# Optimization experiments

Measured on AMD Instinct MI355X. Metric: run time of the kernel, lower is better.

Reference implementation:

```python
import jax, jax.numpy as jnp
import numpy as np

N = 64           # protein_length
B = 32           # batch
L = 2 * N - 1    # lattice side = 127


def setup_inputs() -> dict:
    key = jax.random.key(0)
    k1, k2, k3 = jax.random.split(key, 3)
    acids = jax.random.normal(k1, (B, N), dtype=jnp.float32)
    # raw indices in [0, N-1]; after +(N-1) shift they land in [N-1, 2N-2] < L
    idx = jax.random.randint(k2, (B, N, 3), 0, N, dtype=jnp.int32)
    mask = jax.random.bernoulli(k3, 0.7, (B, N))
    return {"acids": acids, "idx": idx, "mask": mask}


def reference(acids, idx, mask):
    # acids: (B,N) f32, idx: (B,N,3) int, mask: (B,N) bool
    shifted = idx + (N - 1)                       # center lattice at N-1
    vals = jnp.where(mask, acids, jnp.float32(0)) # masked-off acids scatter 0 (no-op under add)
    b = jnp.broadcast_to(jnp.arange(B)[:, None], (B, N))
    lattice = jnp.zeros((B, L, L, L), dtype=jnp.float32)
    # single fused batched scatter (replaces per-sample tf.map_fn + sparse_to_dense)
    lattice = lattice.at[b, shifted[..., 0], shifted[..., 1], shifted[..., 2]].add(vals)
    return lattice
```

## Files before the change

### kernel.cpp

```cpp
#include <hip/hip_runtime.h>


constexpr int PN = 64;
constexpr int PB = 32;
constexpr int PL = 2 * PN - 1;
constexpr long long TOTAL_F = (long long)PB * PL * PL * PL;
constexpr long long TOTAL_V4 = TOTAL_F / 4;
constexpr int NPTS = PB * PN;

constexpr int ZB = 256;
constexpr int ZGRID = 256;
constexpr int CH = (int)((TOTAL_V4 + ZGRID - 1) / ZGRID);

typedef float v4f __attribute__((ext_vector_type(4)));

__global__ __launch_bounds__(ZB) void lattice_fused_kernel(
        const float* __restrict__ acids,
        const int*   __restrict__ idx,
        const int*   __restrict__ mask,
        float*       __restrict__ outf) {
    __shared__ int   s_cnt;
    __shared__ int   s_off[NPTS];
    __shared__ float s_val[NPTS];

    v4f* __restrict__ out = (v4f*)outf;
    const int tid = threadIdx.x;
    const long long lo = (long long)blockIdx.x * CH;
    long long hi = lo + CH;
    if (hi > TOTAL_V4) hi = TOTAL_V4;
    if (tid == 0) s_cnt = 0;
    __syncthreads();

    const long long elo = lo * 4, ehi = hi * 4;
    for (int p = tid; p < NPTS; p += ZB) {
        if (mask[p] != 0) {
            long long b  = (long long)(p >> 6);
            long long i0 = idx[3 * p + 0] + (PN - 1);
            long long i1 = idx[3 * p + 1] + (PN - 1);
            long long i2 = idx[3 * p + 2] + (PN - 1);
            long long off = ((b * PL + i0) * PL + i1) * PL + i2;
            if (off >= elo && off < ehi) {
                int slot = atomicAdd(&s_cnt, 1);
                s_off[slot] = (int)off;
                s_val[slot] = acids[p];
            }
        }
    }

    const v4f z = {0.f, 0.f, 0.f, 0.f};
    for (long long t = lo + tid; t < hi; t += ZB) {
        out[t] = z;
    }

    __syncthreads();
    const int n = s_cnt;
    for (int k = tid; k < n; k += ZB) {
        atomicAdd(outf + s_off[k], s_val[k]);
    }
}

extern "C" void kernel_launch(void* const* d_in, const int* in_sizes, int n_in,
                              void* d_out, int out_size, void* d_ws, size_t ws_size,
                              hipStream_t stream) {
    const float* acids = (const float*)d_in[0];
    const int*   idx   = (const int*)  d_in[1];
    const int*   mask  = (const int*)  d_in[2];
    float* out = (float*)d_out;

    lattice_fused_kernel<<<ZGRID, ZB, 0, stream>>>(acids, idx, mask, out);
}
```

Before: 260.9 us.

## Raise grid size, switch to 32-bit indexing, and unroll zero-fill stores

Increases the block count from 256 to 2048 so the zero-fill of the lattice is spread over more workgroups across the GPU's compute units. It also replaces 64-bit index arithmetic with 32-bit, which is safe because the total element count stays under the int range. The fill loop is unrolled by 8 to issue more independent vector stores per iteration. In exchange, every block still rescans all 2048 points, so that redundant per-block scan grows eightfold.

```diff
diff --git a/kernel.cpp b/kernel.cpp
--- a/kernel.cpp
+++ b/kernel.cpp
@@ -4,13 +4,14 @@
 constexpr int PN = 64;
 constexpr int PB = 32;
 constexpr int PL = 2 * PN - 1;
-constexpr long long TOTAL_F = (long long)PB * PL * PL * PL;
-constexpr long long TOTAL_V4 = TOTAL_F / 4;
+constexpr int TOTAL_F  = PB * PL * PL * PL;
+constexpr int TOTAL_V4 = TOTAL_F / 4;
 constexpr int NPTS = PB * PN;
 
 constexpr int ZB = 256;
-constexpr int ZGRID = 256;
-constexpr int CH = (int)((TOTAL_V4 + ZGRID - 1) / ZGRID);
+constexpr int ZGRID = 2048;
+constexpr int CH = (TOTAL_V4 + ZGRID - 1) / ZGRID;
+constexpr int UNROLL = 8;
 
 typedef float v4f __attribute__((ext_vector_type(4)));
 
@@ -25,32 +26,38 @@
 
     v4f* __restrict__ out = (v4f*)outf;
     const int tid = threadIdx.x;
-    const long long lo = (long long)blockIdx.x * CH;
-    long long hi = lo + CH;
+    const int lo = blockIdx.x * CH;
+    int hi = lo + CH;
     if (hi > TOTAL_V4) hi = TOTAL_V4;
     if (tid == 0) s_cnt = 0;
     __syncthreads();
 
-    const long long elo = lo * 4, ehi = hi * 4;
+    const int elo = lo * 4, ehi = hi * 4;
     for (int p = tid; p < NPTS; p += ZB) {
         if (mask[p] != 0) {
-            long long b  = (long long)(p >> 6);
-            long long i0 = idx[3 * p + 0] + (PN - 1);
-            long long i1 = idx[3 * p + 1] + (PN - 1);
-            long long i2 = idx[3 * p + 2] + (PN - 1);
-            long long off = ((b * PL + i0) * PL + i1) * PL + i2;
+            int b  = p >> 6;
+            int i0 = idx[3 * p + 0] + (PN - 1);
+            int i1 = idx[3 * p + 1] + (PN - 1);
+            int i2 = idx[3 * p + 2] + (PN - 1);
+            int off = ((b * PL + i0) * PL + i1) * PL + i2;
             if (off >= elo && off < ehi) {
                 int slot = atomicAdd(&s_cnt, 1);
-                s_off[slot] = (int)off;
+                s_off[slot] = off;
                 s_val[slot] = acids[p];
             }
         }
     }
 
     const v4f z = {0.f, 0.f, 0.f, 0.f};
-    for (long long t = lo + tid; t < hi; t += ZB) {
+    int t = lo + tid;
+    constexpr int STEP = ZB * UNROLL;
+    for (; t + (UNROLL - 1) * ZB < hi; t += STEP) {
+#pragma unroll
+        for (int u = 0; u < UNROLL; ++u)
+            out[t + u * ZB] = z;
+    }
+    for (; t < hi; t += ZB)
         out[t] = z;
-    }
 
     __syncthreads();
     const int n = s_cnt;
```

New measurement: 264.2 us. About the same (+1.3%).
